# Optimization experiments

Measured on AMD Instinct MI355X. Metric: run time of the kernel, lower is better.

## Reference

```python
import jax, jax.numpy as jnp
import numpy as np

N_NODES = 100000
N_EDGES = 1600000
IN_DIM, H1, H2, OUT_DIM = 256, 128, 64, 32
EPS = 1e-12  # tf.nn.l2_normalize epsilon


def setup_inputs() -> dict:
    key = jax.random.key(0)
    ks = jax.random.split(key, 8)
    features = jax.random.normal(ks[0], (N_NODES, IN_DIM), dtype=jnp.float32)
    edge_vals = jax.random.uniform(ks[1], (N_EDGES,), dtype=jnp.float32)
    # Glorot-uniform weights as in glorot()
    def glorot(k, shape):
        r = np.sqrt(6.0 / (shape[0] + shape[1]))
        return jax.random.uniform(k, shape, minval=-r, maxval=r, dtype=jnp.float32)
    W0 = glorot(ks[2], (IN_DIM, H1))
    W1 = glorot(ks[3], (H1, H2))
    W2 = glorot(ks[4], (H2, OUT_DIM))
    edge_row = jax.random.randint(ks[5], (N_EDGES,), 0, N_NODES, dtype=jnp.int32)
    edge_col = jax.random.randint(ks[6], (N_EDGES,), 0, N_NODES, dtype=jnp.int32)
    return {"features": features, "edge_vals": edge_vals, "W0": W0, "W1": W1,
            "W2": W2, "edge_row": edge_row, "edge_col": edge_col}


def reference(features, edge_vals, W0, W1, W2, edge_row, edge_col):
    # tf.nn.l2_normalize(features, axis=1)
    sq = jnp.sum(features * features, axis=1, keepdims=True)
    x = features * jax.lax.rsqrt(jnp.maximum(sq, EPS))

    def spmm(h):  # support @ h, support sparse in COO form
        msgs = edge_vals[:, None] * h[edge_col]           # [E, d]
        return jax.ops.segment_sum(msgs, edge_row, num_segments=N_NODES)

    h = jax.nn.relu(spmm(x @ W0))      # layer 1
    h = jax.nn.relu(spmm(h @ W1))      # layer 2
    out = spmm(h @ W2)                 # layer 3, identity act
    return out
```

## Files before the change

kernel.cpp:

```cpp
#include <hip/hip_runtime.h>


constexpr int IN_DIM = 256, HD1 = 128, HD2 = 64, OUT_DIM = 32;
constexpr int P1B = 256;

typedef __bf16 bf16x8 __attribute__((ext_vector_type(8)));
typedef float f32x4 __attribute__((ext_vector_type(4)));

__device__ inline ushort f32_to_bf16(float x) {
    unsigned u = __float_as_uint(x);
    unsigned r = (u + 0x7fff + ((u >> 16) & 1)) >> 16;
    return (ushort)r;
}

__device__ inline void unpack_bf16x2(unsigned u, float& lo, float& hi) {
    lo = __uint_as_float(u << 16);
    hi = __uint_as_float(u & 0xffff0000u);
}

__global__ __launch_bounds__(256) void l2norm_kernel(const float* __restrict__ in,
                                                     ushort* __restrict__ out, int M) {
    int wave = threadIdx.x >> 6;
    int lane = threadIdx.x & 63;
    int row = blockIdx.x * 4 + wave;
    if (row >= M) return;
    const float4 v = *reinterpret_cast<const float4*>(&in[(size_t)row * IN_DIM + lane * 4]);
    float s = v.x * v.x + v.y * v.y + v.z * v.z + v.w * v.w;
    #pragma unroll
    for (int off = 32; off; off >>= 1) s += __shfl_xor(s, off, 64);
    float scale = 1.0f / sqrtf(fmaxf(s, 1e-12f));
    uint2 pk;
    pk.x = (unsigned)f32_to_bf16(v.x * scale) | ((unsigned)f32_to_bf16(v.y * scale) << 16);
    pk.y = (unsigned)f32_to_bf16(v.z * scale) | ((unsigned)f32_to_bf16(v.w * scale) << 16);
    *reinterpret_cast<uint2*>(&out[(size_t)row * IN_DIM + lane * 4]) = pk;
}

__global__ __launch_bounds__(256) void wt_kernel(const float* __restrict__ W,
                                                 ushort* __restrict__ WT, int K, int N) {
    int idx = blockIdx.x * 256 + threadIdx.x;
    if (idx < K * N) {
        int k = idx / N, n = idx % N;
        WT[(size_t)n * K + k] = f32_to_bf16(W[idx]);
    }
}


__global__ __launch_bounds__(256) void bucket_count(const int* __restrict__ row,
                                                    int* __restrict__ blockcnt,
                                                    int E, int nbuk, int epb) {
    __shared__ int cnt[512];
    for (int i = threadIdx.x; i < nbuk; i += 256) cnt[i] = 0;
    __syncthreads();
    const int base = blockIdx.x * epb;
    const int end = min(E, base + epb);
    for (int e = base + threadIdx.x; e < end; e += 256)
        atomicAdd(&cnt[row[e] >> 8], 1);
    __syncthreads();
    for (int i = threadIdx.x; i < nbuk; i += 256)
        blockcnt[i * P1B + blockIdx.x] = cnt[i];
}

__global__ __launch_bounds__(256) void scan_bucket_blocks(const int* __restrict__ blockcnt,
                                                          int* __restrict__ blockoff,
                                                          int* __restrict__ bucketcnt) {
    __shared__ int sm[256];
    const int b = blockIdx.x, tid = threadIdx.x;
    const int v = blockcnt[b * P1B + tid];
    sm[tid] = v;
    __syncthreads();
    #pragma unroll
    for (int off = 1; off < 256; off <<= 1) {
        int t = (tid >= off) ? sm[tid - off] : 0;
        __syncthreads();
        sm[tid] += t;
        __syncthreads();
    }
    blockoff[b * P1B + tid] = sm[tid] - v;
    if (tid == 255) bucketcnt[b] = sm[255];
}

__global__ __launch_bounds__(512) void scan_bucket_base(const int* __restrict__ bucketcnt,
                                                        int* __restrict__ bucket_base, int nbuk) {
    __shared__ int sm[512];
    const int tid = threadIdx.x;
    const int v = (tid < nbuk) ? bucketcnt[tid] : 0;
    sm[tid] = v;
    __syncthreads();
    #pragma unroll
    for (int off = 1; off < 512; off <<= 1) {
        int t = (tid >= off) ? sm[tid - off] : 0;
        __syncthreads();
        sm[tid] += t;
        __syncthreads();
    }
    if (tid < nbuk) bucket_base[tid] = sm[tid] - v;
    if (tid == 511) bucket_base[nbuk] = sm[511];
}

__global__ __launch_bounds__(256) void bucket_place(const int* __restrict__ row,
                                                    const int* __restrict__ col,
                                                    const float* __restrict__ val,
                                                    const int* __restrict__ blockoff,
                                                    const int* __restrict__ bucket_base,
                                                    int2* __restrict__ ebuf,
                                                    int E, int nbuk, int epb) {
    __shared__ int pos[512];
    for (int i = threadIdx.x; i < nbuk; i += 256)
        pos[i] = bucket_base[i] + blockoff[i * P1B + blockIdx.x];
    __syncthreads();
    const int base = blockIdx.x * epb;
    const int end = min(E, base + epb);
    for (int e = base + threadIdx.x; e < end; e += 256) {
        int r = row[e];
        int b = r >> 8;
        int p = atomicAdd(&pos[b], 1);
        ebuf[p] = make_int2(col[e] | ((r & 255) << 17), __float_as_int(val[e]));
    }
}

__global__ __launch_bounds__(256) void bucket_csr(const int2* __restrict__ ebuf,
                                                  const int* __restrict__ bucket_base,
                                                  int2* __restrict__ pairs,
                                                  int* __restrict__ row_ptr,
                                                  int M, int nbuk) {
    __shared__ int cnt[256];
    __shared__ int pos[256];
    const int b = blockIdx.x, tid = threadIdx.x;
    const int start = bucket_base[b], end = bucket_base[b + 1];
    cnt[tid] = 0;
    __syncthreads();
    for (int j = start + tid; j < end; j += 256)
        atomicAdd(&cnt[(ebuf[j].x >> 17) & 255], 1);
    __syncthreads();
    const int v = cnt[tid];
    pos[tid] = v;
    __syncthreads();
    #pragma unroll
    for (int off = 1; off < 256; off <<= 1) {
        int t = (tid >= off) ? pos[tid - off] : 0;
        __syncthreads();
        pos[tid] += t;
        __syncthreads();
    }
    const int excl = pos[tid] - v;
    const int rg = b * 256 + tid;
    if (rg < M) row_ptr[rg] = start + excl;
    if (rg == M) row_ptr[M] = start + excl;
    __syncthreads();
    cnt[tid] = excl;
    __syncthreads();
    for (int j = start + tid; j < end; j += 256) {
        int2 e = ebuf[j];
        int rlow = (e.x >> 17) & 255;
        int p = atomicAdd(&cnt[rlow], 1);
        pairs[start + p] = make_int2(e.x & 0x1FFFF, e.y);
    }
}

template <int BN, int WM, int WN>
__global__ __launch_bounds__(256) void gemm_bf16_mfma(
    const ushort* __restrict__ A, const ushort* __restrict__ BT,
    ushort* __restrict__ C, int K) {
    constexpr int BM = 128, BK = 64;
    constexpr int FM = BM / WM / 16;
    constexpr int FN = BN / WN / 16;
    __shared__ ushort As[BM * BK];
    __shared__ ushort Bs[BN * BK];
    const int tid = threadIdx.x;
    const int lane = tid & 63;
    const int wid = tid >> 6;
    const int wm = wid / WN;
    const int wn = wid % WN;
    const int row0 = blockIdx.x * BM;
    const size_t strideB = (size_t)K * 2;

    f32x4 acc[FM][FN] = {};

    const int lkb = ((lane >> 4) << 4) ^ ((lane & 7) << 4);
    const int laneOff = (lane & 15) * 128 + lkb;

    for (int k0 = 0; k0 < K; k0 += BK) {
        {
            constexpr int per_wave = BM * 128 / 4;
            const char* gbase = (const char*)(A + (size_t)row0 * K);
            #pragma unroll
            for (int i = 0; i < per_wave / 1024; ++i) {
                int o = wid * per_wave + i * 1024 + lane * 16;
                int row = o >> 7;
                int kb = (o & 127) ^ ((row & 7) << 4);
                const char* src = gbase + (size_t)row * strideB + (size_t)k0 * 2 + kb;
                ushort* dst = As + (wid * per_wave + i * 1024) / 2;
                __builtin_amdgcn_global_load_lds(
                    (const __attribute__((address_space(1))) unsigned int*)src,
                    (__attribute__((address_space(3))) unsigned int*)dst, 16, 0, 0);
            }
        }
        {
            constexpr int per_wave = BN * 128 / 4;
            const char* gbase = (const char*)BT;
            #pragma unroll
            for (int i = 0; i < per_wave / 1024; ++i) {
                int o = wid * per_wave + i * 1024 + lane * 16;
                int row = o >> 7;
                int kb = (o & 127) ^ ((row & 7) << 4);
                const char* src = gbase + (size_t)row * strideB + (size_t)k0 * 2 + kb;
                ushort* dst = Bs + (wid * per_wave + i * 1024) / 2;
                __builtin_amdgcn_global_load_lds(
                    (const __attribute__((address_space(1))) unsigned int*)src,
                    (__attribute__((address_space(3))) unsigned int*)dst, 16, 0, 0);
            }
        }
        __syncthreads();

        #pragma unroll
        for (int w = 0; w < BK / 32; ++w) {
            bf16x8 af[FM], bfr[FN];
            #pragma unroll
            for (int mi = 0; mi < FM; ++mi) {
                int byte = wm * FM * 2048 + mi * 2048 + (laneOff ^ (w << 6));
                af[mi] = *(const bf16x8*)((const char*)As + byte);
            }
            #pragma unroll
            for (int ni = 0; ni < FN; ++ni) {
                int byte = wn * FN * 2048 + ni * 2048 + (laneOff ^ (w << 6));
                bfr[ni] = *(const bf16x8*)((const char*)Bs + byte);
            }
            #pragma unroll
            for (int mi = 0; mi < FM; ++mi)
                #pragma unroll
                for (int ni = 0; ni < FN; ++ni)
                    acc[mi][ni] = __builtin_amdgcn_mfma_f32_16x16x32_bf16(
                        af[mi], bfr[ni], acc[mi][ni], 0, 0, 0);
        }
        __syncthreads();
    }

    #pragma unroll
    for (int mi = 0; mi < FM; ++mi) {
        #pragma unroll
        for (int ni = 0; ni < FN; ++ni) {
            int rbase = row0 + wm * FM * 16 + mi * 16 + ((lane >> 4) << 2);
            int col = wn * FN * 16 + ni * 16 + (lane & 15);
            #pragma unroll
            for (int r = 0; r < 4; ++r)
                C[(size_t)(rbase + r) * BN + col] = f32_to_bf16(acc[mi][ni][r]);
        }
    }
}

template <int D, bool RELU, bool OUTF32>
__global__ __launch_bounds__(256) void spmm_bf16(const int* __restrict__ row_ptr,
                                                 const int2* __restrict__ pairs,
                                                 const ushort* __restrict__ H,
                                                 void* __restrict__ outp, int M) {
    constexpr int TPR = D / 8;
    const int rpb = 256 / TPR;
    const int lg = threadIdx.x % TPR;
    const int rloc = threadIdx.x / TPR;
    int r = blockIdx.x * rpb + rloc;
    if (r >= M) return;
    const int jb = row_ptr[r], je = row_ptr[r + 1];
    float acc[8] = {};
    int j = jb;
    for (; j + 1 < je; j += 2) {
        int2 p0 = pairs[j];
        int2 p1 = pairs[j + 1];
        uint4 u0 = *reinterpret_cast<const uint4*>(&H[(size_t)p0.x * D + lg * 8]);
        uint4 u1 = *reinterpret_cast<const uint4*>(&H[(size_t)p1.x * D + lg * 8]);
        float v0 = __int_as_float(p0.y), v1 = __int_as_float(p1.y);
        float f[8];
        unpack_bf16x2(u0.x, f[0], f[1]); unpack_bf16x2(u0.y, f[2], f[3]);
        unpack_bf16x2(u0.z, f[4], f[5]); unpack_bf16x2(u0.w, f[6], f[7]);
        #pragma unroll
        for (int i = 0; i < 8; ++i) acc[i] = fmaf(v0, f[i], acc[i]);
        unpack_bf16x2(u1.x, f[0], f[1]); unpack_bf16x2(u1.y, f[2], f[3]);
        unpack_bf16x2(u1.z, f[4], f[5]); unpack_bf16x2(u1.w, f[6], f[7]);
        #pragma unroll
        for (int i = 0; i < 8; ++i) acc[i] = fmaf(v1, f[i], acc[i]);
    }
    if (j < je) {
        int2 p0 = pairs[j];
        uint4 u0 = *reinterpret_cast<const uint4*>(&H[(size_t)p0.x * D + lg * 8]);
        float v0 = __int_as_float(p0.y);
        float f[8];
        unpack_bf16x2(u0.x, f[0], f[1]); unpack_bf16x2(u0.y, f[2], f[3]);
        unpack_bf16x2(u0.z, f[4], f[5]); unpack_bf16x2(u0.w, f[6], f[7]);
        #pragma unroll
        for (int i = 0; i < 8; ++i) acc[i] = fmaf(v0, f[i], acc[i]);
    }
    if (RELU) {
        #pragma unroll
        for (int i = 0; i < 8; ++i) acc[i] = fmaxf(acc[i], 0.f);
    }
    if (OUTF32) {
        float* dst = (float*)outp + (size_t)r * D + lg * 8;
        *reinterpret_cast<float4*>(dst) = *reinterpret_cast<const float4*>(&acc[0]);
        *reinterpret_cast<float4*>(dst + 4) = *reinterpret_cast<const float4*>(&acc[4]);
    } else {
        uint4 pk;
        pk.x = (unsigned)f32_to_bf16(acc[0]) | ((unsigned)f32_to_bf16(acc[1]) << 16);
        pk.y = (unsigned)f32_to_bf16(acc[2]) | ((unsigned)f32_to_bf16(acc[3]) << 16);
        pk.z = (unsigned)f32_to_bf16(acc[4]) | ((unsigned)f32_to_bf16(acc[5]) << 16);
        pk.w = (unsigned)f32_to_bf16(acc[6]) | ((unsigned)f32_to_bf16(acc[7]) << 16);
        *reinterpret_cast<uint4*>((ushort*)outp + (size_t)r * D + lg * 8) = pk;
    }
}

extern "C" void kernel_launch(void* const* d_in, const int* in_sizes, int n_in,
                              void* d_out, int out_size, void* d_ws, size_t ws_size,
                              hipStream_t stream) {
    const float* features  = (const float*)d_in[0];
    const float* edge_vals = (const float*)d_in[1];
    const float* W0        = (const float*)d_in[2];
    const float* W1        = (const float*)d_in[3];
    const float* W2        = (const float*)d_in[4];
    const int*   edge_row  = (const int*)d_in[5];
    const int*   edge_col  = (const int*)d_in[6];
    const int M = in_sizes[0] / IN_DIM;
    const int E = in_sizes[1];
    const int Mp = ((M + 127) / 128) * 128;
    const int nbuk = (M + 255) >> 8;
    const int epb = (E + P1B - 1) / P1B;

    char* ws = (char*)d_ws;
    size_t o = 0;
    auto alloc = [&](size_t bytes) {
        size_t r = o;
        o += (bytes + 1023) & ~(size_t)1023;
        return r;
    };
    ushort* XH      = (ushort*)(ws + alloc((size_t)Mp * IN_DIM * 2));
    ushort* T       = (ushort*)(ws + alloc((size_t)Mp * HD1 * 2));
    int*   rowptr   = (int*)(ws + alloc((size_t)(M + 2) * 4));
    int2*  pairs    = (int2*)(ws + alloc((size_t)E * 8));
    int2*  ebuf     = (int2*)(ws + alloc((size_t)E * 8));
    int*   blockcnt = (int*)(ws + alloc((size_t)512 * P1B * 4));
    int*   blockoff = (int*)(ws + alloc((size_t)512 * P1B * 4));
    int*   bucketcnt= (int*)(ws + alloc((size_t)512 * 4));
    int*   bucketbase=(int*)(ws + alloc((size_t)513 * 4));
    ushort* W0T     = (ushort*)(ws + alloc((size_t)HD1 * IN_DIM * 2));
    ushort* W1T     = (ushort*)(ws + alloc((size_t)HD2 * HD1 * 2));
    ushort* W2T     = (ushort*)(ws + alloc((size_t)OUT_DIM * HD2 * 2));
    float* out = (float*)d_out;
    (void)ws_size; (void)n_in; (void)out_size;

    bucket_count<<<P1B, 256, 0, stream>>>(edge_row, blockcnt, E, nbuk, epb);
    scan_bucket_blocks<<<nbuk, 256, 0, stream>>>(blockcnt, blockoff, bucketcnt);
    scan_bucket_base<<<1, 512, 0, stream>>>(bucketcnt, bucketbase, nbuk);
    bucket_place<<<P1B, 256, 0, stream>>>(edge_row, edge_col, edge_vals,
                                          blockoff, bucketbase, ebuf, E, nbuk, epb);
    bucket_csr<<<nbuk, 256, 0, stream>>>(ebuf, bucketbase, pairs, rowptr, M, nbuk);

    wt_kernel<<<(IN_DIM * HD1 + 255) / 256, 256, 0, stream>>>(W0, W0T, IN_DIM, HD1);
    wt_kernel<<<(HD1 * HD2 + 255) / 256, 256, 0, stream>>>(W1, W1T, HD1, HD2);
    wt_kernel<<<(HD2 * OUT_DIM + 255) / 256, 256, 0, stream>>>(W2, W2T, HD2, OUT_DIM);

    l2norm_kernel<<<(M + 3) / 4, 256, 0, stream>>>(features, XH, M);

    const int gblk = Mp / 128;

    gemm_bf16_mfma<128, 2, 2><<<gblk, 256, 0, stream>>>(XH, W0T, T, IN_DIM);
    spmm_bf16<128, true, false><<<(M + 15) / 16, 256, 0, stream>>>(rowptr, pairs, T, XH, M);

    gemm_bf16_mfma<64, 2, 2><<<gblk, 256, 0, stream>>>(XH, W1T, T, HD1);
    spmm_bf16<64, true, false><<<(M + 31) / 32, 256, 0, stream>>>(rowptr, pairs, T, XH, M);

    gemm_bf16_mfma<32, 4, 1><<<gblk, 256, 0, stream>>>(XH, W2T, T, HD2);
    spmm_bf16<32, false, true><<<(M + 63) / 64, 256, 0, stream>>>(rowptr, pairs, T, out, M);
}
```

Measured before the change: 413.3 us.

## Process each CSR row with a full wavefront and merge weight transposes

Each SpMM row now gets a whole 64-lane wave. Lanes are split into edge groups that gather different neighbours in parallel, and the partial sums are combined with a shuffle-xor reduction. This aims to expose more memory-level parallelism per row, since average degree is about 16, while the old layout had a few lanes walk edges serially. The three weight-transpose launches are also merged into one kernel to cut launch overhead. The costs are padded or clamped wasted loads on ragged tails, shuffle reduction work, and idle lanes at the store.

```diff
diff --git a/kernel.cpp b/kernel.cpp
--- a/kernel.cpp
+++ b/kernel.cpp
@@ -35,12 +35,24 @@
     *reinterpret_cast<uint2*>(&out[(size_t)row * IN_DIM + lane * 4]) = pk;
 }
 
-__global__ __launch_bounds__(256) void wt_kernel(const float* __restrict__ W,
-                                                 ushort* __restrict__ WT, int K, int N) {
+__global__ __launch_bounds__(256) void wt_all(const float* __restrict__ W0,
+                                              const float* __restrict__ W1,
+                                              const float* __restrict__ W2,
+                                              ushort* __restrict__ W0T,
+                                              ushort* __restrict__ W1T,
+                                              ushort* __restrict__ W2T) {
     int idx = blockIdx.x * 256 + threadIdx.x;
-    if (idx < K * N) {
-        int k = idx / N, n = idx % N;
-        WT[(size_t)n * K + k] = f32_to_bf16(W[idx]);
+    if (idx < IN_DIM * HD1) {
+        int k = idx / HD1, n = idx % HD1;
+        W0T[(size_t)n * IN_DIM + k] = f32_to_bf16(W0[idx]);
+    } else if (idx < IN_DIM * HD1 + HD1 * HD2) {
+        int i = idx - IN_DIM * HD1;
+        int k = i / HD2, n = i % HD2;
+        W1T[(size_t)n * HD1 + k] = f32_to_bf16(W1[i]);
+    } else if (idx < IN_DIM * HD1 + HD1 * HD2 + HD2 * OUT_DIM) {
+        int i = idx - IN_DIM * HD1 - HD1 * HD2;
+        int k = i / OUT_DIM, n = i % OUT_DIM;
+        W2T[(size_t)n * HD2 + k] = f32_to_bf16(W2[i]);
     }
 }
 
@@ -249,25 +261,28 @@
 }
 
 template <int D, bool RELU, bool OUTF32>
-__global__ __launch_bounds__(256) void spmm_bf16(const int* __restrict__ row_ptr,
+__global__ __launch_bounds__(256) void spmm_wave(const int* __restrict__ row_ptr,
                                                  const int2* __restrict__ pairs,
                                                  const ushort* __restrict__ H,
                                                  void* __restrict__ outp, int M) {
-    constexpr int TPR = D / 8;
-    const int rpb = 256 / TPR;
-    const int lg = threadIdx.x % TPR;
-    const int rloc = threadIdx.x / TPR;
-    int r = blockIdx.x * rpb + rloc;
+    constexpr int LPE = D / 8;
+    constexpr int EPW = 64 / LPE;
+    const int wv = threadIdx.x >> 6;
+    const int lane = threadIdx.x & 63;
+    const int eg = lane / LPE;
+    const int li = lane % LPE;
+    const int r = blockIdx.x * 4 + wv;
     if (r >= M) return;
     const int jb = row_ptr[r], je = row_ptr[r + 1];
     float acc[8] = {};
-    int j = jb;
-    for (; j + 1 < je; j += 2) {
-        int2 p0 = pairs[j];
-        int2 p1 = pairs[j + 1];
-        uint4 u0 = *reinterpret_cast<const uint4*>(&H[(size_t)p0.x * D + lg * 8]);
-        uint4 u1 = *reinterpret_cast<const uint4*>(&H[(size_t)p1.x * D + lg * 8]);
-        float v0 = __int_as_float(p0.y), v1 = __int_as_float(p1.y);
+    for (int base = jb; base < je; base += 2 * EPW) {
+        int j0 = base + eg, j1 = base + EPW + eg;
+        int2 p0 = pairs[min(j0, je - 1)];
+        int2 p1 = pairs[min(j1, je - 1)];
+        float v0 = (j0 < je) ? __int_as_float(p0.y) : 0.f;
+        float v1 = (j1 < je) ? __int_as_float(p1.y) : 0.f;
+        uint4 u0 = *reinterpret_cast<const uint4*>(&H[(size_t)p0.x * D + li * 8]);
+        uint4 u1 = *reinterpret_cast<const uint4*>(&H[(size_t)p1.x * D + li * 8]);
         float f[8];
         unpack_bf16x2(u0.x, f[0], f[1]); unpack_bf16x2(u0.y, f[2], f[3]);
         unpack_bf16x2(u0.z, f[4], f[5]); unpack_bf16x2(u0.w, f[6], f[7]);
@@ -278,22 +293,17 @@
         #pragma unroll
         for (int i = 0; i < 8; ++i) acc[i] = fmaf(v1, f[i], acc[i]);
     }
-    if (j < je) {
-        int2 p0 = pairs[j];
-        uint4 u0 = *reinterpret_cast<const uint4*>(&H[(size_t)p0.x * D + lg * 8]);
-        float v0 = __int_as_float(p0.y);
-        float f[8];
-        unpack_bf16x2(u0.x, f[0], f[1]); unpack_bf16x2(u0.y, f[2], f[3]);
-        unpack_bf16x2(u0.z, f[4], f[5]); unpack_bf16x2(u0.w, f[6], f[7]);
-        #pragma unroll
-        for (int i = 0; i < 8; ++i) acc[i] = fmaf(v0, f[i], acc[i]);
-    }
+    #pragma unroll
+    for (int off = LPE; off < 64; off <<= 1)
+        #pragma unroll
+        for (int i = 0; i < 8; ++i) acc[i] += __shfl_xor(acc[i], off, 64);
+    if (eg != 0) return;
     if (RELU) {
         #pragma unroll
         for (int i = 0; i < 8; ++i) acc[i] = fmaxf(acc[i], 0.f);
     }
     if (OUTF32) {
-        float* dst = (float*)outp + (size_t)r * D + lg * 8;
+        float* dst = (float*)outp + (size_t)r * D + li * 8;
         *reinterpret_cast<float4*>(dst) = *reinterpret_cast<const float4*>(&acc[0]);
         *reinterpret_cast<float4*>(dst + 4) = *reinterpret_cast<const float4*>(&acc[4]);
     } else {
@@ -302,7 +312,7 @@
         pk.y = (unsigned)f32_to_bf16(acc[2]) | ((unsigned)f32_to_bf16(acc[3]) << 16);
         pk.z = (unsigned)f32_to_bf16(acc[4]) | ((unsigned)f32_to_bf16(acc[5]) << 16);
         pk.w = (unsigned)f32_to_bf16(acc[6]) | ((unsigned)f32_to_bf16(acc[7]) << 16);
-        *reinterpret_cast<uint4*>((ushort*)outp + (size_t)r * D + lg * 8) = pk;
+        *reinterpret_cast<uint4*>((ushort*)outp + (size_t)r * D + li * 8) = pk;
     }
 }
 
@@ -351,20 +361,20 @@
                                           blockoff, bucketbase, ebuf, E, nbuk, epb);
     bucket_csr<<<nbuk, 256, 0, stream>>>(ebuf, bucketbase, pairs, rowptr, M, nbuk);
 
-    wt_kernel<<<(IN_DIM * HD1 + 255) / 256, 256, 0, stream>>>(W0, W0T, IN_DIM, HD1);
-    wt_kernel<<<(HD1 * HD2 + 255) / 256, 256, 0, stream>>>(W1, W1T, HD1, HD2);
-    wt_kernel<<<(HD2 * OUT_DIM + 255) / 256, 256, 0, stream>>>(W2, W2T, HD2, OUT_DIM);
+    wt_all<<<(IN_DIM * HD1 + HD1 * HD2 + HD2 * OUT_DIM + 255) / 256, 256, 0, stream>>>(
+        W0, W1, W2, W0T, W1T, W2T);
 
     l2norm_kernel<<<(M + 3) / 4, 256, 0, stream>>>(features, XH, M);
 
     const int gblk = Mp / 128;
+    const int sblk = (M + 3) / 4;
 
     gemm_bf16_mfma<128, 2, 2><<<gblk, 256, 0, stream>>>(XH, W0T, T, IN_DIM);
-    spmm_bf16<128, true, false><<<(M + 15) / 16, 256, 0, stream>>>(rowptr, pairs, T, XH, M);
+    spmm_wave<128, true, false><<<sblk, 256, 0, stream>>>(rowptr, pairs, T, XH, M);
 
     gemm_bf16_mfma<64, 2, 2><<<gblk, 256, 0, stream>>>(XH, W1T, T, HD1);
-    spmm_bf16<64, true, false><<<(M + 31) / 32, 256, 0, stream>>>(rowptr, pairs, T, XH, M);
+    spmm_wave<64, true, false><<<sblk, 256, 0, stream>>>(rowptr, pairs, T, XH, M);
 
     gemm_bf16_mfma<32, 4, 1><<<gblk, 256, 0, stream>>>(XH, W2T, T, HD2);
-    spmm_bf16<32, false, true><<<(M + 63) / 64, 256, 0, stream>>>(rowptr, pairs, T, out, M);
-}
+    spmm_wave<32, false, true><<<sblk, 256, 0, stream>>>(rowptr, pairs, T, out, M);
+}
```

After: 409.8 us. About the same (-0.8%).
